# Kernel optimization log

Hardware: AMD Instinct MI355X
Metric: run time of the kernel (lower is better)

Reference implementation:

```python
import jax, jax.numpy as jnp
import numpy as np

B, N, D, H = 4, 2048, 768, 12
HD = D // H
SCALE = HD ** -0.5


def setup_inputs() -> dict:
    key = jax.random.key(0)
    k1, k2, k3 = jax.random.split(key, 3)
    x = jax.random.normal(k1, (B, N, D), dtype=jnp.float32)
    w_qkv = jax.random.normal(k2, (D, 3 * D), dtype=jnp.float32) * (D ** -0.5)
    w_proj = jax.random.normal(k3, (D, D), dtype=jnp.float32) * (D ** -0.5)
    b_proj = jnp.zeros((D,), dtype=jnp.float32)
    return {"x": x, "w_qkv": w_qkv, "w_proj": w_proj, "b_proj": b_proj}


def reference(x, w_qkv, w_proj, b_proj):
    b, n, d = x.shape
    qkv = x @ w_qkv                      # [b, n, 3d]
    q, k, v = jnp.split(qkv, 3, axis=-1)
    # [b, n, d] -> [b, h, n, hd]
    split_heads = lambda t: t.reshape(b, n, H, HD).transpose(0, 2, 1, 3)
    q, k, v = split_heads(q), split_heads(k), split_heads(v)
    dots = jnp.einsum('bhqd,bhkd->bhqk', q, k) * SCALE   # [b, h, n, n]
    attn = jax.nn.softmax(dots, axis=-1)
    q_attn = attn[:, :, 0, :]            # attention row of query token 0: [b, h, n]
    # dropout p=0 (eval) -> identity
    out = jnp.einsum('bhqk,bhkd->bhqd', attn, v)          # [b, h, n, hd]
    out = out.transpose(0, 2, 1, 3).reshape(b, n, d)      # [b, n, d]
    return out @ w_proj + b_proj, q_attn
```

## Files before the change

kernel.cpp:

```cpp
#include <hip/hip_runtime.h>


typedef unsigned short u16;
typedef __attribute__((ext_vector_type(8))) short bf8;
typedef __attribute__((ext_vector_type(4))) short bf4;
typedef __attribute__((ext_vector_type(4))) float f4;

#define MFMA16(a, b, c) __builtin_amdgcn_mfma_f32_16x16x32_bf16((a), (b), (c), 0, 0, 0)

#if __has_builtin(__builtin_amdgcn_exp2f)
#define EXP2(x) __builtin_amdgcn_exp2f(x)
#else
#define EXP2(x) __expf((x) * 0.6931471805599453f)
#endif

__device__ __forceinline__ float b2f(u16 h) {
  union { unsigned u; float f; } v; v.u = ((unsigned)h) << 16; return v.f;
}
__device__ __forceinline__ u16 f2b(float f) {
  union { float f; unsigned u; } v; v.f = f;
  unsigned r = v.u + 0x7fffu + ((v.u >> 16) & 1u);
  return (u16)(r >> 16);
}
__device__ __forceinline__ u16 f2bt(float f) {
  union { float f; unsigned u; } v; v.f = f;
  return (u16)(v.u >> 16);
}
__device__ __forceinline__ void gload16(const u16* g, u16* l) {
  __builtin_amdgcn_global_load_lds(
      (const __attribute__((address_space(1))) void*)g,
      (__attribute__((address_space(3))) void*)l, 16, 0, 0);
}
__device__ __forceinline__ int detect_f32(const u16* x) {
  unsigned v = x[2 * (threadIdx.x & 63)];
  unsigned e = (v >> 7) & 0xFF;
  return __ballot(e >= 0x8E) != 0ull;
}

__global__ __launch_bounds__(256) void convert_bf16(
    const void* __restrict__ in, u16* __restrict__ out, int n) {
  const int f32 = detect_f32((const u16*)in);
  for (int i = blockIdx.x * 256 + threadIdx.x; i < n; i += gridDim.x * 256)
    out[i] = f32 ? f2b(((const float*)in)[i]) : ((const u16*)in)[i];
}

__global__ __launch_bounds__(256) void transpose_two(
    const void* __restrict__ wqkv, u16* __restrict__ wqkvT,
    const void* __restrict__ wproj, u16* __restrict__ wprojT,
    const u16* __restrict__ xdet) {
  const int z = blockIdx.z;
  if (z == 1 && blockIdx.x >= 24) return;
  const void* in = z ? wproj : wqkv;
  u16* out = z ? wprojT : wqkvT;
  const int R = 768, C = z ? 768 : 2304;
  __shared__ u16 tile[32][33];
  const int f32 = detect_f32(xdet);
  const int bx = blockIdx.x * 32;
  const int by = blockIdx.y * 32;
  const int tx = threadIdx.x & 31, ty = threadIdx.x >> 5;
#pragma unroll
  for (int i = 0; i < 4; i++) {
    size_t idx = (size_t)(by + ty + i * 8) * C + bx + tx;
    tile[ty + i * 8][tx] = f32 ? f2b(((const float*)in)[idx]) : ((const u16*)in)[idx];
  }
  __syncthreads();
#pragma unroll
  for (int i = 0; i < 4; i++)
    out[(size_t)(bx + ty + i * 8) * R + by + tx] = tile[tx][ty + i * 8];
}

template <int BIAS>
__global__ __launch_bounds__(256, 4) void gemm_bt(
    const u16* __restrict__ A, const u16* __restrict__ Bt,
    const void* __restrict__ bias, void* __restrict__ C,
    int M, int Ncols, int K, const u16* __restrict__ xdet,
    u16* __restrict__ Vt) {
  __shared__ alignas(16) u16 Al[2][128 * 32];
  __shared__ alignas(16) u16 Bl[2][128 * 32];
  const int t = threadIdx.x;
  const int lane = t & 63, wave = t >> 6;
  const int wr = wave >> 1, wc = wave & 1;
  const int quad = lane >> 4, l16 = lane & 15;
  const int bm = blockIdx.y * 128, bn = blockIdx.x * 128;
  const int f32o = BIAS ? detect_f32(xdet) : 0;
  const int grow = lane >> 2, gcol = (lane & 3) * 8;
  const int chunk0 = wave * 2, chunk1 = wave * 2 + 1;
  const int arow0 = chunk0 * 16 + grow, arow1 = chunk1 * 16 + grow;
  f4 acc[4][4] = {};
  gload16(A + (size_t)(bm + arow0) * K + gcol, &Al[0][chunk0 * 512]);
  gload16(Bt + (size_t)(bn + arow0) * K + gcol, &Bl[0][chunk0 * 512]);
  gload16(A + (size_t)(bm + arow1) * K + gcol, &Al[0][chunk1 * 512]);
  gload16(Bt + (size_t)(bn + arow1) * K + gcol, &Bl[0][chunk1 * 512]);
  const int NIT = K >> 5;
  for (int i = 0; i < NIT; i++) {
    const int cur = i & 1, nxt = cur ^ 1;
    __syncthreads();
    if (i + 1 < NIT) {
      int k0 = (i + 1) << 5;
      gload16(A + (size_t)(bm + arow0) * K + k0 + gcol, &Al[nxt][chunk0 * 512]);
      gload16(Bt + (size_t)(bn + arow0) * K + k0 + gcol, &Bl[nxt][chunk0 * 512]);
      gload16(A + (size_t)(bm + arow1) * K + k0 + gcol, &Al[nxt][chunk1 * 512]);
      gload16(Bt + (size_t)(bn + arow1) * K + k0 + gcol, &Bl[nxt][chunk1 * 512]);
    }
    bf8 af[4], bfr[4];
#pragma unroll
    for (int mt = 0; mt < 4; mt++)
      af[mt] = *(const bf8*)&Al[cur][(wr * 64 + mt * 16 + l16) * 32 + quad * 8];
#pragma unroll
    for (int nt = 0; nt < 4; nt++)
      bfr[nt] = *(const bf8*)&Bl[cur][(wc * 64 + nt * 16 + l16) * 32 + quad * 8];
#pragma unroll
    for (int mt = 0; mt < 4; mt++)
#pragma unroll
      for (int nt = 0; nt < 4; nt++)
        acc[mt][nt] = MFMA16(af[mt], bfr[nt], acc[mt][nt]);
  }
  if (Vt != nullptr && bn >= 1536) {
    const int b = bm >> 11;
#pragma unroll
    for (int mt = 0; mt < 4; mt++) {
      int n0 = (bm & 2047) + wr * 64 + mt * 16 + quad * 4;
      int n2 = (n0 & ~31) | (((n0 >> 2) & 3) << 3) | (((n0 >> 4) & 1) << 2);
#pragma unroll
      for (int nt = 0; nt < 4; nt++) {
        int colv = bn - 1536 + wc * 64 + nt * 16 + l16;
        int h = colv >> 6, d = colv & 63;
        bf4 pk = {(short)f2b(acc[mt][nt][0]), (short)f2b(acc[mt][nt][1]),
                  (short)f2b(acc[mt][nt][2]), (short)f2b(acc[mt][nt][3])};
        *(bf4*)&Vt[(size_t)((b * 12 + h) * 64 + d) * 2048 + n2] = pk;
      }
    }
    return;
  }
#pragma unroll
  for (int mt = 0; mt < 4; mt++) {
    int row = bm + wr * 64 + mt * 16 + quad * 4;
#pragma unroll
    for (int nt = 0; nt < 4; nt++) {
      int col = bn + wc * 64 + nt * 16 + l16;
      float bv = 0.f;
      if (BIAS)
        bv = f32o ? ((const float*)bias)[col] : b2f(((const u16*)bias)[col]);
#pragma unroll
      for (int r = 0; r < 4; r++) {
        size_t idx = (size_t)(row + r) * Ncols + col;
        float v = acc[mt][nt][r] + bv;
        if (f32o) ((float*)C)[idx] = v; else ((u16*)C)[idx] = f2b(v);
      }
    }
  }
}

__global__ __launch_bounds__(256, 3) void flash_attn(
    const u16* __restrict__ qkv, const u16* __restrict__ Vt,
    u16* __restrict__ O, float* __restrict__ qe, float* __restrict__ lout) {
  const int STR = 72;
  __shared__ alignas(16) u16 Kl[2][64 * 72];
  __shared__ alignas(16) u16 Vl[2][64 * 72];
  const int t = threadIdx.x, lane = t & 63, wave = t >> 6;
  const int quad = lane >> 4, l16 = lane & 15;
  const int id = blockIdx.x;
  const int bh = (id & 7) + 8 * (id >> 7);
  const int qtile = (id >> 3) & 15;
  const int b = bh / 12, h = bh - b * 12;
  const int q0 = qtile * 128 + wave * 32;
  const bool dumpP = (qe != nullptr) && (qtile == 0) && (wave == 0);
  const float SCALE2 = 0.125f * 1.44269504089f;
  const float mM0 = -16.f;
  bf8 qf[2][2];
#pragma unroll
  for (int qt = 0; qt < 2; qt++) {
    const u16* Qr = qkv + (size_t)(b * 2048 + q0 + qt * 16 + l16) * 2304 + h * 64;
    bf8 r0 = *(const bf8*)(Qr + quad * 8);
    bf8 r1 = *(const bf8*)(Qr + 32 + quad * 8);
#pragma unroll
    for (int j = 0; j < 8; j++) {
      qf[qt][0][j] = (short)f2b(b2f((u16)r0[j]) * SCALE2);
      qf[qt][1][j] = (short)f2b(b2f((u16)r1[j]) * SCALE2);
    }
  }
  const u16* Kb = qkv + (size_t)(b * 2048) * 2304 + 768 + h * 64;
  const u16* Vb = Vt + (size_t)((b * 12 + h) * 64) * 2048;
  const int srow = t >> 3, sc8 = (t & 7) * 8;
  const int srow2 = srow + 32;
  f4 o[2][4] = {};
  float lpart[2] = {0.f, 0.f};

  bf8 kreg0 = *(const bf8*)(Kb + (size_t)srow * 2304 + sc8);
  bf8 kreg1 = *(const bf8*)(Kb + (size_t)srow2 * 2304 + sc8);
  bf8 vreg0 = *(const bf8*)(Vb + (size_t)srow * 2048 + sc8);
  bf8 vreg1 = *(const bf8*)(Vb + (size_t)srow2 * 2048 + sc8);
  *(bf8*)&Kl[0][srow * STR + sc8] = kreg0;
  *(bf8*)&Kl[0][srow2 * STR + sc8] = kreg1;
  *(bf8*)&Vl[0][srow * STR + sc8] = vreg0;
  *(bf8*)&Vl[0][srow2 * STR + sc8] = vreg1;
  {
    const u16* Kn = Kb + (size_t)64 * 2304;
    const u16* Vn = Vb + 64;
    kreg0 = *(const bf8*)(Kn + (size_t)srow * 2304 + sc8);
    kreg1 = *(const bf8*)(Kn + (size_t)srow2 * 2304 + sc8);
    vreg0 = *(const bf8*)(Vn + (size_t)srow * 2048 + sc8);
    vreg1 = *(const bf8*)(Vn + (size_t)srow2 * 2048 + sc8);
  }

  for (int i = 0; i < 32; i++) {
    const int cur = i & 1, nxt = cur ^ 1;
    __syncthreads();
    bf8 pf[2][2];
#pragma unroll
    for (int kt = 0; kt < 4; kt++) {
      bf8 kf0 = *(const bf8*)&Kl[cur][(kt * 16 + l16) * STR + quad * 8];
      bf8 kf1 = *(const bf8*)&Kl[cur][(kt * 16 + l16) * STR + 32 + quad * 8];
#pragma unroll
      for (int qt = 0; qt < 2; qt++) {
        f4 z = {mM0, mM0, mM0, mM0};
        z = MFMA16(kf0, qf[qt][0], z);
        z = MFMA16(kf1, qf[qt][1], z);
        float e0 = EXP2(z[0]);
        float e1 = EXP2(z[1]);
        float e2 = EXP2(z[2]);
        float e3 = EXP2(z[3]);
        lpart[qt] += (e0 + e1) + (e2 + e3);
        if (qt == 0 && dumpP && l16 == 0) {
          f4 ev = {e0, e1, e2, e3};
          *(f4*)&qe[bh * 2048 + i * 64 + kt * 16 + quad * 4] = ev;
        }
        pf[qt][kt >> 1][(kt & 1) * 4 + 0] = (short)f2bt(e0);
        pf[qt][kt >> 1][(kt & 1) * 4 + 1] = (short)f2bt(e1);
        pf[qt][kt >> 1][(kt & 1) * 4 + 2] = (short)f2bt(e2);
        pf[qt][kt >> 1][(kt & 1) * 4 + 3] = (short)f2bt(e3);
      }
    }
#pragma unroll
    for (int pair = 0; pair < 2; pair++) {
#pragma unroll
      for (int nt = 0; nt < 4; nt++) {
        bf8 vf = *(const bf8*)&Vl[cur][(nt * 16 + l16) * STR + pair * 32 + quad * 8];
        o[0][nt] = MFMA16(vf, pf[0][pair], o[0][nt]);
        o[1][nt] = MFMA16(vf, pf[1][pair], o[1][nt]);
      }
    }
    if (i + 1 < 32) {
      *(bf8*)&Kl[nxt][srow * STR + sc8] = kreg0;
      *(bf8*)&Kl[nxt][srow2 * STR + sc8] = kreg1;
      *(bf8*)&Vl[nxt][srow * STR + sc8] = vreg0;
      *(bf8*)&Vl[nxt][srow2 * STR + sc8] = vreg1;
    }
    if (i + 2 < 32) {
      const u16* Kn = Kb + (size_t)(i * 64 + 128) * 2304;
      const u16* Vn = Vb + (i * 64 + 128);
      kreg0 = *(const bf8*)(Kn + (size_t)srow * 2304 + sc8);
      kreg1 = *(const bf8*)(Kn + (size_t)srow2 * 2304 + sc8);
      vreg0 = *(const bf8*)(Vn + (size_t)srow * 2048 + sc8);
      vreg1 = *(const bf8*)(Vn + (size_t)srow2 * 2048 + sc8);
    }
  }
#pragma unroll
  for (int qt = 0; qt < 2; qt++) {
    float l = lpart[qt];
    l += __shfl_xor(l, 16, 64);
    l += __shfl_xor(l, 32, 64);
    if (qt == 0 && dumpP && lane == 0) lout[bh] = l;
    float inv = 1.f / l;
    size_t row = (size_t)(b * 2048 + q0 + qt * 16 + l16) * 768 + h * 64;
#pragma unroll
    for (int nt = 0; nt < 4; nt++) {
      bf4 pk = {(short)f2b(o[qt][nt][0] * inv), (short)f2b(o[qt][nt][1] * inv),
                (short)f2b(o[qt][nt][2] * inv), (short)f2b(o[qt][nt][3] * inv)};
      *(bf4*)&O[row + nt * 16 + quad * 4] = pk;
    }
  }
}

__global__ __launch_bounds__(256) void qattn_norm(
    const float* __restrict__ qe, const float* __restrict__ lout,
    void* __restrict__ out, const u16* __restrict__ xdet) {
  const int bh = blockIdx.x;
  const int f32o = detect_f32(xdet);
  const float inv = 1.f / lout[bh];
  for (int k = threadIdx.x; k < 2048; k += 256) {
    size_t idx = (size_t)6291456 + (size_t)bh * 2048 + k;
    float v = qe[bh * 2048 + k] * inv;
    if (f32o) ((float*)out)[idx] = v; else ((u16*)out)[idx] = f2b(v);
  }
}

__global__ __launch_bounds__(256) void qattn_row0(
    const u16* __restrict__ qkv, void* __restrict__ out,
    const u16* __restrict__ xdet) {
  const int bh = blockIdx.x, b = bh / 12, h = bh % 12;
  __shared__ float qs[64];
  __shared__ float sv[2048];
  __shared__ float red[8];
  const int t = threadIdx.x;
  const int f32o = detect_f32(xdet);
  if (t < 64) qs[t] = b2f(qkv[(size_t)(b * 2048) * 2304 + h * 64 + t]);
  __syncthreads();
  float lmax = -1e30f;
  for (int k = t; k < 2048; k += 256) {
    const u16* Kr = qkv + (size_t)(b * 2048 + k) * 2304 + 768 + h * 64;
    float acc = 0.f;
#pragma unroll
    for (int j = 0; j < 8; j++) {
      bf8 kv = *(const bf8*)(Kr + j * 8);
#pragma unroll
      for (int d = 0; d < 8; d++) acc += qs[j * 8 + d] * b2f((u16)kv[d]);
    }
    acc *= 0.125f;
    sv[k] = acc;
    lmax = fmaxf(lmax, acc);
  }
#pragma unroll
  for (int off = 32; off >= 1; off >>= 1) lmax = fmaxf(lmax, __shfl_xor(lmax, off, 64));
  if ((t & 63) == 0) red[t >> 6] = lmax;
  __syncthreads();
  const float bmax = fmaxf(fmaxf(red[0], red[1]), fmaxf(red[2], red[3]));
  float lsum = 0.f;
  for (int k = t; k < 2048; k += 256) {
    float e = __expf(sv[k] - bmax);
    sv[k] = e;
    lsum += e;
  }
#pragma unroll
  for (int off = 32; off >= 1; off >>= 1) lsum += __shfl_xor(lsum, off, 64);
  if ((t & 63) == 0) red[4 + (t >> 6)] = lsum;
  __syncthreads();
  const float inv = 1.f / (red[4] + red[5] + red[6] + red[7]);
  for (int k = t; k < 2048; k += 256) {
    size_t idx = (size_t)6291456 + (size_t)bh * 2048 + k;
    float v = sv[k] * inv;
    if (f32o) ((float*)out)[idx] = v; else ((u16*)out)[idx] = f2b(v);
  }
}

extern "C" void kernel_launch(void* const* d_in, const int* in_sizes, int n_in,
                              void* d_out, int out_size, void* d_ws, size_t ws_size,
                              hipStream_t stream) {
  const void* x_raw      = d_in[0];
  const void* w_qkv_raw  = d_in[1];
  const void* w_proj_raw = d_in[2];
  const void* b_proj_raw = d_in[3];
  const u16* xdet = (const u16*)x_raw;
  char* ws = (char*)d_ws;
  u16* xbf    = (u16*)(ws + 256);
  u16* wqkvT  = (u16*)(ws + 12583168);
  u16* wprojT = (u16*)(ws + 16122112);
  u16* qkv    = (u16*)(ws + 17301760);
  u16* Vt     = (u16*)(ws + 55050496);
  float* qe   = (float*)(ws + 67633408);
  float* lout = (float*)(ws + 68026624);
  u16* attn   = xbf;
  const bool fused = ws_size >= 68026816ull;

  convert_bf16<<<2048, 256, 0, stream>>>(x_raw, xbf, 6291456);
  transpose_two<<<dim3(72, 24, 2), 256, 0, stream>>>(
      w_qkv_raw, wqkvT, w_proj_raw, wprojT, xdet);
  gemm_bt<0><<<dim3(18, 64), 256, 0, stream>>>(
      xbf, wqkvT, nullptr, qkv, 8192, 2304, 768, xdet, Vt);
  flash_attn<<<dim3(768), 256, 0, stream>>>(qkv, Vt, attn,
                                            fused ? qe : nullptr,
                                            fused ? lout : nullptr);
  if (fused)
    qattn_norm<<<dim3(48), 256, 0, stream>>>(qe, lout, d_out, xdet);
  else
    qattn_row0<<<dim3(48), 256, 0, stream>>>(qkv, d_out, xdet);
  gemm_bt<1><<<dim3(6, 64), 256, 0, stream>>>(
      attn, wprojT, b_proj_raw, d_out, 8192, 768, 768, xdet, nullptr);
}
```

Before: 227.9 us.

## Fuse prep kernels, async LDS loads in flash attention, fold qattn norm into proj GEMM

The x conversion and both weight transposes now run in a single prep launch, and the x conversion is vectorised to process element pairs. The flash attention kernel stages K/V tiles with global_load_lds straight into an unpadded LDS layout instead of going through registers, and packs P to bf16 with a byte-permute. The query-0 attention normalisation moves into extra blocks of the output-projection GEMM, which removes one launch. The aim is fewer launches and less register and VMEM-to-LDS staging overhead. The risk is LDS bank conflicts, since the 32-element row stride has no padding.

```diff
diff --git a/kernel.cpp b/kernel.cpp
--- a/kernel.cpp
+++ b/kernel.cpp
@@ -4,6 +4,7 @@
 typedef unsigned short u16;
 typedef __attribute__((ext_vector_type(8))) short bf8;
 typedef __attribute__((ext_vector_type(4))) short bf4;
+typedef __attribute__((ext_vector_type(4))) int i4;
 typedef __attribute__((ext_vector_type(4))) float f4;
 
 #define MFMA16(a, b, c) __builtin_amdgcn_mfma_f32_16x16x32_bf16((a), (b), (c), 0, 0, 0)
@@ -22,9 +23,14 @@
   unsigned r = v.u + 0x7fffu + ((v.u >> 16) & 1u);
   return (u16)(r >> 16);
 }
-__device__ __forceinline__ u16 f2bt(float f) {
-  union { float f; unsigned u; } v; v.f = f;
-  return (u16)(v.u >> 16);
+__device__ __forceinline__ unsigned pack2(float a, float b) {
+#if __has_builtin(__builtin_amdgcn_perm)
+  return __builtin_amdgcn_perm(__builtin_bit_cast(unsigned, b),
+                               __builtin_bit_cast(unsigned, a), 0x07060302u);
+#else
+  return (__builtin_bit_cast(unsigned, b) & 0xFFFF0000u) |
+         (__builtin_bit_cast(unsigned, a) >> 16);
+#endif
 }
 __device__ __forceinline__ void gload16(const u16* g, u16* l) {
   __builtin_amdgcn_global_load_lds(
@@ -37,26 +43,36 @@
   return __ballot(e >= 0x8E) != 0ull;
 }
 
-__global__ __launch_bounds__(256) void convert_bf16(
-    const void* __restrict__ in, u16* __restrict__ out, int n) {
-  const int f32 = detect_f32((const u16*)in);
-  for (int i = blockIdx.x * 256 + threadIdx.x; i < n; i += gridDim.x * 256)
-    out[i] = f32 ? f2b(((const float*)in)[i]) : ((const u16*)in)[i];
-}
-
-__global__ __launch_bounds__(256) void transpose_two(
+__global__ __launch_bounds__(256) void prep(
+    const void* __restrict__ x, u16* __restrict__ xbf,
     const void* __restrict__ wqkv, u16* __restrict__ wqkvT,
-    const void* __restrict__ wproj, u16* __restrict__ wprojT,
-    const u16* __restrict__ xdet) {
+    const void* __restrict__ wproj, u16* __restrict__ wprojT) {
   const int z = blockIdx.z;
+  if (z == 2) {
+    const int f32 = detect_f32((const u16*)x);
+    const int lin = blockIdx.y * 72 + blockIdx.x;
+    if (f32) {
+      const float2* in = (const float2*)x;
+      unsigned* out = (unsigned*)xbf;
+      for (int i = lin * 256 + threadIdx.x; i < 3145728; i += 442368) {
+        float2 v = in[i];
+        out[i] = (unsigned)f2b(v.x) | ((unsigned)f2b(v.y) << 16);
+      }
+    } else {
+      const unsigned* in = (const unsigned*)x;
+      unsigned* out = (unsigned*)xbf;
+      for (int i = lin * 256 + threadIdx.x; i < 3145728; i += 442368)
+        out[i] = in[i];
+    }
+    return;
+  }
   if (z == 1 && blockIdx.x >= 24) return;
   const void* in = z ? wproj : wqkv;
   u16* out = z ? wprojT : wqkvT;
   const int R = 768, C = z ? 768 : 2304;
   __shared__ u16 tile[32][33];
-  const int f32 = detect_f32(xdet);
-  const int bx = blockIdx.x * 32;
-  const int by = blockIdx.y * 32;
+  const int f32 = detect_f32((const u16*)x);
+  const int bx = blockIdx.x * 32, by = blockIdx.y * 32;
   const int tx = threadIdx.x & 31, ty = threadIdx.x >> 5;
 #pragma unroll
   for (int i = 0; i < 4; i++) {
@@ -69,12 +85,24 @@
     out[(size_t)(bx + ty + i * 8) * R + by + tx] = tile[tx][ty + i * 8];
 }
 
-template <int BIAS>
+template <int BIAS, int QATTN>
 __global__ __launch_bounds__(256, 4) void gemm_bt(
     const u16* __restrict__ A, const u16* __restrict__ Bt,
     const void* __restrict__ bias, void* __restrict__ C,
     int M, int Ncols, int K, const u16* __restrict__ xdet,
-    u16* __restrict__ Vt) {
+    u16* __restrict__ Vt, const float* __restrict__ qe,
+    const float* __restrict__ lout) {
+  if (QATTN && blockIdx.x == 6) {
+    const int f32o = detect_f32(xdet);
+    const int base = blockIdx.y * 1536;
+    for (int j = threadIdx.x; j < 1536; j += 256) {
+      int idx = base + j;
+      float v = qe[idx] * (1.f / lout[idx >> 11]);
+      size_t oidx = (size_t)6291456 + idx;
+      if (f32o) ((float*)C)[oidx] = v; else ((u16*)C)[oidx] = f2b(v);
+    }
+    return;
+  }
   __shared__ alignas(16) u16 Al[2][128 * 32];
   __shared__ alignas(16) u16 Bl[2][128 * 32];
   const int t = threadIdx.x;
@@ -154,9 +182,7 @@
 __global__ __launch_bounds__(256, 3) void flash_attn(
     const u16* __restrict__ qkv, const u16* __restrict__ Vt,
     u16* __restrict__ O, float* __restrict__ qe, float* __restrict__ lout) {
-  const int STR = 72;
-  __shared__ alignas(16) u16 Kl[2][64 * 72];
-  __shared__ alignas(16) u16 Vl[2][64 * 72];
+  __shared__ alignas(16) u16 lds[2][8192];
   const int t = threadIdx.x, lane = t & 63, wave = t >> 6;
   const int quad = lane >> 4, l16 = lane & 15;
   const int id = blockIdx.x;
@@ -181,36 +207,41 @@
   }
   const u16* Kb = qkv + (size_t)(b * 2048) * 2304 + 768 + h * 64;
   const u16* Vb = Vt + (size_t)((b * 12 + h) * 64) * 2048;
-  const int srow = t >> 3, sc8 = (t & 7) * 8;
-  const int srow2 = srow + 32;
+  const int drow = wave * 16 + (lane >> 2);
+  const int dcol = (lane & 3) * 8;
   f4 o[2][4] = {};
   float lpart[2] = {0.f, 0.f};
 
-  bf8 kreg0 = *(const bf8*)(Kb + (size_t)srow * 2304 + sc8);
-  bf8 kreg1 = *(const bf8*)(Kb + (size_t)srow2 * 2304 + sc8);
-  bf8 vreg0 = *(const bf8*)(Vb + (size_t)srow * 2048 + sc8);
-  bf8 vreg1 = *(const bf8*)(Vb + (size_t)srow2 * 2048 + sc8);
-  *(bf8*)&Kl[0][srow * STR + sc8] = kreg0;
-  *(bf8*)&Kl[0][srow2 * STR + sc8] = kreg1;
-  *(bf8*)&Vl[0][srow * STR + sc8] = vreg0;
-  *(bf8*)&Vl[0][srow2 * STR + sc8] = vreg1;
   {
-    const u16* Kn = Kb + (size_t)64 * 2304;
-    const u16* Vn = Vb + 64;
-    kreg0 = *(const bf8*)(Kn + (size_t)srow * 2304 + sc8);
-    kreg1 = *(const bf8*)(Kn + (size_t)srow2 * 2304 + sc8);
-    vreg0 = *(const bf8*)(Vn + (size_t)srow * 2048 + sc8);
-    vreg1 = *(const bf8*)(Vn + (size_t)srow2 * 2048 + sc8);
+    const u16* Kt = Kb + (size_t)drow * 2304 + dcol;
+    const u16* Vr = Vb + (size_t)drow * 2048 + dcol;
+    u16* base = &lds[0][wave * 512];
+    gload16(Kt, base);
+    gload16(Kt + 32, base + 2048);
+    gload16(Vr, base + 4096);
+    gload16(Vr + 32, base + 6144);
   }
 
   for (int i = 0; i < 32; i++) {
-    const int cur = i & 1, nxt = cur ^ 1;
+    const int cur = i & 1;
     __syncthreads();
-    bf8 pf[2][2];
+    if (i + 1 < 32) {
+      int n1 = (i + 1) * 64;
+      const u16* Kt = Kb + (size_t)(n1 + drow) * 2304 + dcol;
+      const u16* Vr = Vb + (size_t)drow * 2048 + n1 + dcol;
+      u16* base = &lds[cur ^ 1][wave * 512];
+      gload16(Kt, base);
+      gload16(Kt + 32, base + 2048);
+      gload16(Vr, base + 4096);
+      gload16(Vr + 32, base + 6144);
+    }
+    const u16* K0 = &lds[cur][0];
+    const u16* K1 = &lds[cur][2048];
+    union { i4 i; bf8 b; } pf[2][2];
 #pragma unroll
     for (int kt = 0; kt < 4; kt++) {
-      bf8 kf0 = *(const bf8*)&Kl[cur][(kt * 16 + l16) * STR + quad * 8];
-      bf8 kf1 = *(const bf8*)&Kl[cur][(kt * 16 + l16) * STR + 32 + quad * 8];
+      bf8 kf0 = *(const bf8*)&K0[(kt * 16 + l16) * 32 + quad * 8];
+      bf8 kf1 = *(const bf8*)&K1[(kt * 16 + l16) * 32 + quad * 8];
 #pragma unroll
       for (int qt = 0; qt < 2; qt++) {
         f4 z = {mM0, mM0, mM0, mM0};
@@ -225,34 +256,19 @@
           f4 ev = {e0, e1, e2, e3};
           *(f4*)&qe[bh * 2048 + i * 64 + kt * 16 + quad * 4] = ev;
         }
-        pf[qt][kt >> 1][(kt & 1) * 4 + 0] = (short)f2bt(e0);
-        pf[qt][kt >> 1][(kt & 1) * 4 + 1] = (short)f2bt(e1);
-        pf[qt][kt >> 1][(kt & 1) * 4 + 2] = (short)f2bt(e2);
-        pf[qt][kt >> 1][(kt & 1) * 4 + 3] = (short)f2bt(e3);
+        pf[qt][kt >> 1].i[(kt & 1) * 2 + 0] = (int)pack2(e0, e1);
+        pf[qt][kt >> 1].i[(kt & 1) * 2 + 1] = (int)pack2(e2, e3);
       }
     }
 #pragma unroll
     for (int pair = 0; pair < 2; pair++) {
+      const u16* Vp = &lds[cur][4096 + pair * 2048];
 #pragma unroll
       for (int nt = 0; nt < 4; nt++) {
-        bf8 vf = *(const bf8*)&Vl[cur][(nt * 16 + l16) * STR + pair * 32 + quad * 8];
-        o[0][nt] = MFMA16(vf, pf[0][pair], o[0][nt]);
-        o[1][nt] = MFMA16(vf, pf[1][pair], o[1][nt]);
-      }
-    }
-    if (i + 1 < 32) {
-      *(bf8*)&Kl[nxt][srow * STR + sc8] = kreg0;
-      *(bf8*)&Kl[nxt][srow2 * STR + sc8] = kreg1;
-      *(bf8*)&Vl[nxt][srow * STR + sc8] = vreg0;
-      *(bf8*)&Vl[nxt][srow2 * STR + sc8] = vreg1;
-    }
-    if (i + 2 < 32) {
-      const u16* Kn = Kb + (size_t)(i * 64 + 128) * 2304;
-      const u16* Vn = Vb + (i * 64 + 128);
-      kreg0 = *(const bf8*)(Kn + (size_t)srow * 2304 + sc8);
-      kreg1 = *(const bf8*)(Kn + (size_t)srow2 * 2304 + sc8);
-      vreg0 = *(const bf8*)(Vn + (size_t)srow * 2048 + sc8);
-      vreg1 = *(const bf8*)(Vn + (size_t)srow2 * 2048 + sc8);
+        bf8 vf = *(const bf8*)&Vp[(nt * 16 + l16) * 32 + quad * 8];
+        o[0][nt] = MFMA16(vf, pf[0][pair].b, o[0][nt]);
+        o[1][nt] = MFMA16(vf, pf[1][pair].b, o[1][nt]);
+      }
     }
   }
 #pragma unroll
@@ -269,19 +285,6 @@
                 (short)f2b(o[qt][nt][2] * inv), (short)f2b(o[qt][nt][3] * inv)};
       *(bf4*)&O[row + nt * 16 + quad * 4] = pk;
     }
-  }
-}
-
-__global__ __launch_bounds__(256) void qattn_norm(
-    const float* __restrict__ qe, const float* __restrict__ lout,
-    void* __restrict__ out, const u16* __restrict__ xdet) {
-  const int bh = blockIdx.x;
-  const int f32o = detect_f32(xdet);
-  const float inv = 1.f / lout[bh];
-  for (int k = threadIdx.x; k < 2048; k += 256) {
-    size_t idx = (size_t)6291456 + (size_t)bh * 2048 + k;
-    float v = qe[bh * 2048 + k] * inv;
-    if (f32o) ((float*)out)[idx] = v; else ((u16*)out)[idx] = f2b(v);
   }
 }
 
@@ -352,18 +355,19 @@
   u16* attn   = xbf;
   const bool fused = ws_size >= 68026816ull;
 
-  convert_bf16<<<2048, 256, 0, stream>>>(x_raw, xbf, 6291456);
-  transpose_two<<<dim3(72, 24, 2), 256, 0, stream>>>(
-      w_qkv_raw, wqkvT, w_proj_raw, wprojT, xdet);
-  gemm_bt<0><<<dim3(18, 64), 256, 0, stream>>>(
-      xbf, wqkvT, nullptr, qkv, 8192, 2304, 768, xdet, Vt);
+  prep<<<dim3(72, 24, 3), 256, 0, stream>>>(
+      x_raw, xbf, w_qkv_raw, wqkvT, w_proj_raw, wprojT);
+  gemm_bt<0, 0><<<dim3(18, 64), 256, 0, stream>>>(
+      xbf, wqkvT, nullptr, qkv, 8192, 2304, 768, xdet, Vt, nullptr, nullptr);
   flash_attn<<<dim3(768), 256, 0, stream>>>(qkv, Vt, attn,
                                             fused ? qe : nullptr,
                                             fused ? lout : nullptr);
-  if (fused)
-    qattn_norm<<<dim3(48), 256, 0, stream>>>(qe, lout, d_out, xdet);
-  else
+  if (fused) {
+    gemm_bt<1, 1><<<dim3(7, 64), 256, 0, stream>>>(
+        attn, wprojT, b_proj_raw, d_out, 8192, 768, 768, xdet, nullptr, qe, lout);
+  } else {
+    gemm_bt<1, 0><<<dim3(6, 64), 256, 0, stream>>>(
+        attn, wprojT, b_proj_raw, d_out, 8192, 768, 768, xdet, nullptr, nullptr, nullptr);
     qattn_row0<<<dim3(48), 256, 0, stream>>>(qkv, d_out, xdet);
-  gemm_bt<1><<<dim3(6, 64), 256, 0, stream>>>(
-      attn, wprojT, b_proj_raw, d_out, 8192, 768, 768, xdet, nullptr);
-}
+  }
+}
```

Result: faster. 217.4 us (-4.6%).
